# Kernel tuning notes

Hardware: AMD Instinct MI355X
Metric: run time of the kernel (lower is better)

The kernel has to match this reference:

```python
import jax, jax.numpy as jnp
import numpy as np

EPS = 1e-15

def gmm_conv(x, row, col, pseudo, g_w, mu, sigma, root_w, bias):
    # x: [N,Fin], pseudo: [E,D], g_w: [Fin,K*Fout], mu/sigma: [K,D], root_w: [Fin,Fout]
    N = x.shape[0]
    K, D = mu.shape
    Fout = g_w.shape[1] // K
    gx = (x @ g_w).reshape(N, K, Fout)                       # per-node kernel transforms
    diff = pseudo[:, None, :] - mu[None, :, :]               # [E,K,D]
    gauss = jnp.exp(-0.5 * jnp.sum(diff * diff / (EPS + sigma[None] ** 2), axis=-1))  # [E,K]
    msg = jnp.einsum('ek,eko->eo', gauss, gx[row])           # [E,Fout]
    agg = jax.ops.segment_sum(msg, col, num_segments=N)      # scatter-add to targets
    cnt = jax.ops.segment_sum(jnp.ones((msg.shape[0],), x.dtype), col, num_segments=N)
    agg = agg / jnp.maximum(cnt, 1.0)[:, None]               # mean aggregation (GMMConv default)
    return agg + x @ root_w + bias

def setup_inputs() -> dict:
    key = jax.random.key(0)
    ks = jax.random.split(key, 12)
    N, E, F, H, C, K, D = 50000, 800000, 128, 64, 16, 8, 2
    return {
        'x': jax.random.normal(ks[0], (N, F), jnp.float32),
        'edge_index': jax.random.randint(ks[1], (2, E), 0, N, jnp.int64),
        'edge_attr': jax.random.uniform(ks[2], (E, D), jnp.float32),
        'g1_w': jax.random.normal(ks[3], (F, K * H), jnp.float32) * 0.1,
        'mu1': jax.random.normal(ks[4], (K, D), jnp.float32),
        'sigma1': jax.random.uniform(ks[5], (K, D), jnp.float32) + 0.5,
        'root1_w': jax.random.normal(ks[6], (F, H), jnp.float32) * 0.1,
        'bias1': jnp.zeros((H,), jnp.float32),
        'g2_w': jax.random.normal(ks[7], (H, K * C), jnp.float32) * 0.1,
        'mu2': jax.random.normal(ks[8], (K, D), jnp.float32),
        'sigma2': jax.random.uniform(ks[9], (K, D), jnp.float32) + 0.5,
        'root2_w': jax.random.normal(ks[10], (H, C), jnp.float32) * 0.1,
        'bias2': jnp.zeros((C,), jnp.float32),
    }

def reference(x, edge_index, edge_attr, g1_w, mu1, sigma1, root1_w, bias1,
              g2_w, mu2, sigma2, root2_w, bias2):
    row, col = edge_index[0], edge_index[1]
    # dropout p applied in eval mode -> identity
    h = jax.nn.elu(gmm_conv(x, row, col, edge_attr, g1_w, mu1, sigma1, root1_w, bias1))
    out = gmm_conv(h, row, col, edge_attr, g2_w, mu2, sigma2, root2_w, bias2)
    return jax.nn.log_softmax(out, axis=1)
```

## Files before the change

kernel.cpp:

```cpp
#include <hip/hip_runtime.h>
#include <hip/hip_bf16.h>
#include <hip/hip_fp16.h>
#include <math.h>


#define NF 128
#define NH 64
#define NC 16
#define Z1NODES 16
#define Z1CAP 448
#define E2NODES 16
#define E2CAP 320
#define GXST 160

typedef __bf16 v8bf __attribute__((ext_vector_type(8)));
typedef float v4f __attribute__((ext_vector_type(4)));
typedef float v2f __attribute__((ext_vector_type(2)));

__device__ inline ushort f2bu(float x) {
  __hip_bfloat16 h = __float2bfloat16(x);
  return *(ushort*)&h;
}
__device__ inline uint packh2(float a, float b) {
  __half ha = __float2half_rn(a), hb = __float2half_rn(b);
  return (uint)(*(ushort*)&ha) | ((uint)(*(ushort*)&hb) << 16);
}
__device__ inline float2 unph2(uint u) {
  ushort a = (ushort)(u & 0xffff), b = (ushort)(u >> 16);
  return make_float2(__half2float(*(__half*)&a), __half2float(*(__half*)&b));
}
__device__ inline v8bf ld_frag(const ushort* p) {
  uint4 u = *(const uint4*)p;
  return __builtin_bit_cast(v8bf, u);
}
__device__ inline v2f fma2(float w, v2f f, v2f a) {
  return __builtin_elementwise_fma((v2f){w, w}, f, a);
}

__global__ __launch_bounds__(256) void setup_kernel(
    const int* __restrict__ col, const float* __restrict__ x,
    const float* __restrict__ g1w, const float* __restrict__ r1w,
    const float* __restrict__ g2w, const float* __restrict__ r2w,
    int* __restrict__ counts, ushort* __restrict__ A1,
    ushort* __restrict__ W1t, ushort* __restrict__ G2pT,
    int* __restrict__ bagg, int E, int N, int bh, int bc, int bp) {
  const int b = blockIdx.x, t = threadIdx.x;
  if (b < bh) {
    int e = b * 256 + t;
    if (e < E) atomicAdd(&counts[col[e]], 1);
  } else if (b < bh + bc) {
    int idx = (b - bh) * 256 + t;
    if (idx < N * 32) {
      int n = idx >> 5, c4 = idx & 31;
      float4 v = ((const float4*)x)[idx];
      ushort4 o;
      o.x = f2bu(v.x); o.y = f2bu(v.y); o.z = f2bu(v.z); o.w = f2bu(v.w);
      *(ushort4*)(A1 + (size_t)n * 1152 + 1024 + c4 * 4) = o;
    }
  } else if (b < bh + bc + bp) {
    int i = (b - bh - bc) * 256 + t;
    if (i < 64 * 1152) {
      int h = i / 1152, j = i % 1152;
      float v = (j < 1024) ? g1w[(size_t)(j & 127) * 512 + (j >> 7) * 64 + h]
                           : r1w[(size_t)(j - 1024) * 64 + h];
      W1t[i] = f2bu(v);
    } else {
      int i2 = i - 64 * 1152;
      if (i2 < 144 * 64) {
        int cp = i2 / 64, f = i2 % 64;
        float v;
        if (cp < 128) {
          int kq = cp >> 5, rem = cp & 31;
          int o = rem >> 1, k = kq * 2 + (rem & 1);
          v = g2w[(size_t)f * 128 + k * 16 + o];
        } else {
          v = r2w[(size_t)f * 16 + (cp - 128)];
        }
        G2pT[i2] = f2bu(v);
      }
    }
  } else {
    if (t < 64) bagg[t] = 0;
  }
}

__global__ __launch_bounds__(256) void scan_kernel(
    const int* __restrict__ counts, int* __restrict__ starts,
    int* __restrict__ cursor, int* __restrict__ bagg, int NB) {
  __shared__ int wsum[4];
  __shared__ int s_pre;
  const int t = threadIdx.x, lane = t & 63, wv = t >> 6;
  const int b = blockIdx.x;
  int4 v = ((const int4*)counts)[b * 256 + t];
  int tsum = v.x + v.y + v.z + v.w;
  int inc = tsum;
  #pragma unroll
  for (int off = 1; off < 64; off <<= 1) {
    int u = __shfl_up(inc, off, 64);
    if (lane >= off) inc += u;
  }
  if (lane == 63) wsum[wv] = inc;
  __syncthreads();
  int agg = wsum[0] + wsum[1] + wsum[2] + wsum[3];
  if (t == 0) atomicExch(&bagg[b], agg + 1);
  __threadfence();
  int pre = 0;
  if (wv == 0) {
    if (t < b) {
      int val;
      do { val = atomicAdd(&bagg[t], 0); } while (val == 0);
      pre = val - 1;
    }
    #pragma unroll
    for (int off = 32; off >= 1; off >>= 1) pre += __shfl_xor(pre, off, 64);
    if (lane == 0) s_pre = pre;
  }
  __syncthreads();
  int wpre = 0;
  for (int j = 0; j < wv; ++j) wpre += wsum[j];
  int excl = s_pre + wpre + inc - tsum;
  int4 o;
  o.x = excl; o.y = o.x + v.x; o.z = o.y + v.y; o.w = o.z + v.z;
  ((int4*)starts)[b * 256 + t] = o;
  ((int4*)cursor)[b * 256 + t] = o;
}

__global__ __launch_bounds__(256) void fill_kernel(
    const int* __restrict__ row, const int* __restrict__ col,
    const float* __restrict__ eattr,
    const float* __restrict__ mu1, const float* __restrict__ sg1,
    const float* __restrict__ mu2, const float* __restrict__ sg2,
    int* __restrict__ cursor, int* __restrict__ erow,
    uint4* __restrict__ ew1, uint4* __restrict__ ew2, int E) {
  int e = blockIdx.x * 256 + threadIdx.x;
  if (e >= E) return;
  int c = col[e];
  int pos = atomicAdd(&cursor[c], 1);
  float p0 = eattr[2 * e], p1 = eattr[2 * e + 1];
  float w1[8], w2[8];
  #pragma unroll
  for (int k = 0; k < 8; ++k) {
    float d0 = p0 - mu1[2 * k], d1 = p1 - mu1[2 * k + 1];
    float s0 = sg1[2 * k], s1 = sg1[2 * k + 1];
    w1[k] = __expf(-0.5f * (d0 * d0 / (1e-15f + s0 * s0) +
                            d1 * d1 / (1e-15f + s1 * s1)));
    float e0 = p0 - mu2[2 * k], e1 = p1 - mu2[2 * k + 1];
    float t0 = sg2[2 * k], t1 = sg2[2 * k + 1];
    w2[k] = __expf(-0.5f * (e0 * e0 / (1e-15f + t0 * t0) +
                            e1 * e1 / (1e-15f + t1 * t1)));
  }
  erow[pos] = row[e];
  ew1[pos] = make_uint4(packh2(w1[0], w1[1]), packh2(w1[2], w1[3]),
                        packh2(w1[4], w1[5]), packh2(w1[6], w1[7]));
  ew2[pos] = make_uint4(packh2(w2[0], w2[1]), packh2(w2[2], w2[3]),
                        packh2(w2[4], w2[5]), packh2(w2[6], w2[7]));
}

__global__ __launch_bounds__(256) void z1_kernel(
    ushort* __restrict__ A1, const int* __restrict__ erow,
    const uint4* __restrict__ ew1, const int* __restrict__ starts, int N) {
  __shared__ __align__(16) float lw[Z1CAP + 8][8];
  __shared__ int loff[Z1CAP + 8];
  const int t = threadIdx.x, lane = t & 63, wv = t >> 6;
  const int base = (int)blockIdx.x * Z1NODES;
  const int S = starts[base];
  const int cl = min(starts[base + Z1NODES] - S, Z1CAP);
  for (int i = t; i < cl; i += 256) {
    loff[i] = erow[S + i] * 2304;
    uint4 qq = ew1[S + i];
    float2 a = unph2(qq.x), b = unph2(qq.y), c = unph2(qq.z), d = unph2(qq.w);
    *(float4*)&lw[i][0] = make_float4(a.x, a.y, b.x, b.y);
    *(float4*)&lw[i][4] = make_float4(c.x, c.y, d.x, d.y);
  }
  if (t < 8) {
    loff[cl + t] = 0;
    *(float4*)&lw[cl + t][0] = make_float4(0.f, 0.f, 0.f, 0.f);
    *(float4*)&lw[cl + t][4] = make_float4(0.f, 0.f, 0.f, 0.f);
  }
  __syncthreads();

  const char* xb = (const char*)(A1 + 1024) + (lane << 2);

  for (int i = 0; i < Z1NODES / 4; ++i) {
    const int n = base + wv * 4 + i;
    const int be = starts[n], ee = starts[n + 1];
    v2f A[8];
    #pragma unroll
    for (int k = 0; k < 8; ++k) A[k] = (v2f){0.f, 0.f};

    const int reRel = min(ee - S, cl);
    for (int q = min(be - S, cl); q < reRel; q += 8) {
      int off[8];
      #pragma unroll
      for (int u = 0; u < 8; ++u) off[u] = loff[q + u];
      uint g[8];
      #pragma unroll
      for (int u = 0; u < 8; ++u) g[u] = *(const uint*)(xb + off[u]);
      #pragma unroll
      for (int u = 0; u < 8; ++u) {
        const bool ok = (q + u) < reRel;
        float4 wl = *(float4*)&lw[q + u][0];
        float4 wh = *(float4*)&lw[q + u][4];
        v2f F;
        F.x = ok ? __uint_as_float(g[u] << 16) : 0.f;
        F.y = ok ? __uint_as_float(g[u] & 0xffff0000u) : 0.f;
        A[0] = fma2(wl.x, F, A[0]);
        A[1] = fma2(wl.y, F, A[1]);
        A[2] = fma2(wl.z, F, A[2]);
        A[3] = fma2(wl.w, F, A[3]);
        A[4] = fma2(wh.x, F, A[4]);
        A[5] = fma2(wh.y, F, A[5]);
        A[6] = fma2(wh.z, F, A[6]);
        A[7] = fma2(wh.w, F, A[7]);
      }
    }
    for (int j = max(S + reRel, be); j < ee; ++j) {
      uint4 qq = ew1[j];
      uint g = *(const uint*)(xb + erow[j] * 2304);
      float2 a = unph2(qq.x), b = unph2(qq.y), c = unph2(qq.z), d = unph2(qq.w);
      v2f F;
      F.x = __uint_as_float(g << 16);
      F.y = __uint_as_float(g & 0xffff0000u);
      A[0] = fma2(a.x, F, A[0]); A[1] = fma2(a.y, F, A[1]);
      A[2] = fma2(b.x, F, A[2]); A[3] = fma2(b.y, F, A[3]);
      A[4] = fma2(c.x, F, A[4]); A[5] = fma2(c.y, F, A[5]);
      A[6] = fma2(d.x, F, A[6]); A[7] = fma2(d.y, F, A[7]);
    }
    const float inv = 1.f / fmaxf((float)(ee - be), 1.f);
    ushort* zr = A1 + (size_t)n * 1152;
    #pragma unroll
    for (int k = 0; k < 8; ++k) {
      uint pk = (uint)f2bu(A[k].x * inv) | ((uint)f2bu(A[k].y * inv) << 16);
      *(uint*)(zr + k * 128 + 2 * lane) = pk;
    }
  }
}

__global__ __launch_bounds__(256) void gemm12_kernel(
    const ushort* __restrict__ A1, const ushort* __restrict__ W1t,
    const float* __restrict__ b1, const ushort* __restrict__ G2pT,
    ushort* __restrict__ gx2e, int N) {
  __shared__ __align__(16) ushort As[2][64 * 32];
  __shared__ __align__(16) ushort Bs[2][64 * 32];
  __shared__ __align__(16) ushort Hs[64][72];
  const int t = threadIdx.x, lane = t & 63, wv = t >> 6;
  const int mfrag = lane & 15, quad = lane >> 4;
  const int m0 = (int)blockIdx.x * 64;
  const int st_r = t >> 2, st_c = (t & 3) * 8;
  const int st_o = st_r * 32 + st_c;
  const ushort* ag = A1 + (size_t)(m0 + st_r) * 1152 + st_c;
  const ushort* bg = W1t + (size_t)st_r * 1152 + st_c;

  {
    uint4 a0 = *(const uint4*)ag;
    uint4 b0 = *(const uint4*)bg;
    *(uint4*)(&As[0][st_o]) = a0;
    *(uint4*)(&Bs[0][st_o]) = b0;
  }
  __syncthreads();

  v4f acc[4];
  #pragma unroll
  for (int ct = 0; ct < 4; ++ct) acc[ct] = (v4f){0.f, 0.f, 0.f, 0.f};

  for (int kc = 0; kc < 36; ++kc) {
    const int cb = kc & 1, nb = cb ^ 1;
    uint4 an, bn;
    if (kc < 35) {
      an = *(const uint4*)(ag + (kc + 1) * 32);
      bn = *(const uint4*)(bg + (kc + 1) * 32);
    }
    v8bf a = ld_frag(&As[cb][(wv * 16 + mfrag) * 32 + quad * 8]);
    #pragma unroll
    for (int ct = 0; ct < 4; ++ct) {
      v8bf b = ld_frag(&Bs[cb][(ct * 16 + mfrag) * 32 + quad * 8]);
      acc[ct] = __builtin_amdgcn_mfma_f32_16x16x32_bf16(a, b, acc[ct], 0, 0, 0);
    }
    if (kc < 35) {
      *(uint4*)(&As[nb][st_o]) = an;
      *(uint4*)(&Bs[nb][st_o]) = bn;
      __syncthreads();
    }
  }
  #pragma unroll
  for (int ct = 0; ct < 4; ++ct) {
    const int colh = ct * 16 + mfrag;
    const float bc = b1[colh];
    #pragma unroll
    for (int r = 0; r < 4; ++r) {
      float v = acc[ct][r] + bc;
      v = v > 0.f ? v : expm1f(v);
      Hs[wv * 16 + quad * 4 + r][colh] = f2bu(v);
    }
  }
  __syncthreads();

  v4f acc2[9];
  #pragma unroll
  for (int t9 = 0; t9 < 9; ++t9) acc2[t9] = (v4f){0.f, 0.f, 0.f, 0.f};
  const ushort* brow = G2pT + (size_t)mfrag * 64 + quad * 8;
  #pragma unroll
  for (int kc = 0; kc < 2; ++kc) {
    v8bf a = ld_frag(&Hs[wv * 16 + mfrag][quad * 8 + kc * 32]);
    #pragma unroll
    for (int t9 = 0; t9 < 9; ++t9) {
      v8bf b = ld_frag(brow + (size_t)t9 * 16 * 64 + kc * 32);
      acc2[t9] = __builtin_amdgcn_mfma_f32_16x16x32_bf16(a, b, acc2[t9], 0, 0, 0);
    }
  }
  #pragma unroll
  for (int t9 = 0; t9 < 9; ++t9) {
    #pragma unroll
    for (int r = 0; r < 4; ++r) {
      int node = m0 + wv * 16 + quad * 4 + r;
      if (node < N)
        gx2e[(size_t)node * GXST + t9 * 16 + mfrag] = f2bu(acc2[t9][r]);
    }
  }
}

__global__ __launch_bounds__(256) void edge2_kernel(
    const ushort* __restrict__ gx2e, const int* __restrict__ erow,
    const uint4* __restrict__ ew2, const int* __restrict__ starts,
    const float* __restrict__ b2, float* __restrict__ out, int N) {
  __shared__ __align__(16) float lw[E2CAP + 8][8];
  __shared__ int loff[E2CAP + 8];
  __shared__ float lb2[16];
  const int t = threadIdx.x, lane = t & 63, wv = t >> 6;
  const int base = (int)blockIdx.x * E2NODES;
  const int S = starts[base];
  const int cl = min(starts[base + E2NODES] - S, E2CAP);
  if (t < 16) lb2[t] = b2[t];
  for (int i = t; i < cl; i += 256) {
    loff[i] = erow[S + i] * 320;
    uint4 qq = ew2[S + i];
    float2 a = unph2(qq.x), b = unph2(qq.y), c = unph2(qq.z), d = unph2(qq.w);
    *(float4*)&lw[i][0] = make_float4(a.x, a.y, b.x, b.y);
    *(float4*)&lw[i][4] = make_float4(c.x, c.y, d.x, d.y);
  }
  if (t < 8) {
    loff[cl + t] = 0;
    *(float4*)&lw[cl + t][0] = make_float4(0.f, 0.f, 0.f, 0.f);
    *(float4*)&lw[cl + t][4] = make_float4(0.f, 0.f, 0.f, 0.f);
  }
  __syncthreads();

  const int o = lane & 15, kq = lane >> 4;
  const char* gb = (const char*)gx2e + kq * 64 + o * 4;

  for (int i = 0; i < E2NODES / 4; ++i) {
    const int n = base + wv * 4 + i;
    if (n >= N) continue;
    const int be = starts[n], ee = starts[n + 1];
    v2f ACC = (v2f){0.f, 0.f};
    const int reRel = min(ee - S, cl);
    for (int q = min(be - S, cl); q < reRel; q += 8) {
      int off[8];
      #pragma unroll
      for (int u = 0; u < 8; ++u) off[u] = loff[q + u];
      uint g[8];
      #pragma unroll
      for (int u = 0; u < 8; ++u) g[u] = *(const uint*)(gb + off[u]);
      #pragma unroll
      for (int u = 0; u < 8; ++u) {
        const bool ok = (q + u) < reRel;
        v2f W = *(v2f*)&lw[q + u][kq * 2];
        v2f F;
        F.x = ok ? __uint_as_float(g[u] << 16) : 0.f;
        F.y = ok ? __uint_as_float(g[u] & 0xffff0000u) : 0.f;
        ACC = __builtin_elementwise_fma(W, F, ACC);
      }
    }
    for (int j = max(S + reRel, be); j < ee; ++j) {
      uint4 qq = ew2[j];
      uint comp = (kq == 0) ? qq.x : (kq == 1) ? qq.y : (kq == 2) ? qq.z : qq.w;
      float2 wp = unph2(comp);
      uint g = *(const uint*)(gb + erow[j] * 320);
      ACC.x = fmaf(wp.x, __uint_as_float(g << 16), ACC.x);
      ACC.y = fmaf(wp.y, __uint_as_float(g & 0xffff0000u), ACC.y);
    }
    float s = ACC.x + ACC.y;
    s += __shfl_xor(s, 16, 64);
    s += __shfl_xor(s, 32, 64);
    const float inv = 1.f / fmaxf((float)(ee - be), 1.f);
    ushort ru = *((const ushort*)gx2e + (size_t)n * GXST + 128 + o);
    float root = __uint_as_float(((uint)ru) << 16);
    float v = s * inv + root + lb2[o];
    float mx = v;
    #pragma unroll
    for (int off = 8; off >= 1; off >>= 1) mx = fmaxf(mx, __shfl_xor(mx, off, 64));
    float sm = __expf(v - mx);
    #pragma unroll
    for (int off = 8; off >= 1; off >>= 1) sm += __shfl_xor(sm, off, 64);
    if (kq == 0) out[(size_t)n * NC + o] = v - mx - __logf(sm);
  }
}

extern "C" void kernel_launch(void* const* d_in, const int* in_sizes, int n_in,
                              void* d_out, int out_size, void* d_ws, size_t ws_size,
                              hipStream_t stream) {
  const float* x     = (const float*)d_in[0];
  const int*   eidx  = (const int*)d_in[1];
  const float* eattr = (const float*)d_in[2];
  const float* g1w   = (const float*)d_in[3];
  const float* mu1   = (const float*)d_in[4];
  const float* sg1   = (const float*)d_in[5];
  const float* r1w   = (const float*)d_in[6];
  const float* b1    = (const float*)d_in[7];
  const float* g2w   = (const float*)d_in[8];
  const float* mu2   = (const float*)d_in[9];
  const float* sg2   = (const float*)d_in[10];
  const float* r2w   = (const float*)d_in[11];
  const float* b2    = (const float*)d_in[12];

  const int N = in_sizes[0] / NF;
  const int E = in_sizes[1] / 2;
  const int* row = eidx;
  const int* col = eidx + E;
  const int N2 = (N + 63) & ~63;
  const int NP = (N + 1023) & ~1023;
  const int NB = NP / 1024;

  char* wsb = (char*)d_ws;
  uint4* ew2   = (uint4*)wsb;
  uint4* ew1   = (uint4*)(wsb + (size_t)E * 16);
  ushort* gx2e = (ushort*)ew1;
  size_t ew1span = (size_t)N2 * 320;
  if (ew1span < (size_t)E * 16) ew1span = (size_t)E * 16;
  ushort* A1   = (ushort*)(wsb + (size_t)E * 16 + ew1span);
  ushort* W1t  = A1 + (size_t)N2 * 1152;
  ushort* G2pT = W1t + (size_t)64 * 1152;
  int* erow    = (int*)(G2pT + (size_t)144 * 64);
  int* counts  = erow + (size_t)E;
  int* starts  = counts + NP;
  int* cursor  = starts + NP;
  int* bagg    = cursor + NP;

  const int bh = (E + 255) / 256;
  const int bc = (N * 32 + 255) / 256;
  const int bp = (64 * 1152 + 144 * 64 + 255) / 256;

  hipMemsetAsync(counts, 0, (size_t)NP * sizeof(int), stream);
  setup_kernel<<<bh + bc + bp + 1, 256, 0, stream>>>(
      col, x, g1w, r1w, g2w, r2w, counts, A1, W1t, G2pT, bagg, E, N, bh, bc, bp);
  scan_kernel<<<NB, 256, 0, stream>>>(counts, starts, cursor, bagg, NB);
  fill_kernel<<<bh, 256, 0, stream>>>(row, col, eattr, mu1, sg1, mu2, sg2,
                                      cursor, erow, ew1, ew2, E);
  z1_kernel<<<N / Z1NODES, 256, 0, stream>>>(A1, erow, ew1, starts, N);
  gemm12_kernel<<<N2 / 64, 256, 0, stream>>>(A1, W1t, b1, G2pT, gx2e, N);
  edge2_kernel<<<(N + E2NODES - 1) / E2NODES, 256, 0, stream>>>(
      gx2e, erow, ew2, starts, b2, (float*)d_out, N);
}
```

Before: 334.6 us.

## Record edge rank in histogram pass and recompute gaussian weights in consumers

The histogram pass now stores each edge's atomic rank, so the fill pass places edges at starts[col]+rank without a second atomic on a cursor array. Fill writes one 16-byte record per edge holding precomputed row offsets for both layers and the raw pseudo-coordinates, instead of separate erow plus two fp16 weight arrays. The z1 and edge2 kernels recompute the 8 gaussian weights on the fly from shared-memory mu/sigma constants. This trades extra exp work in the aggregation kernels for less edge-array traffic and one fewer atomic pass, and keeps the weights in fp32 instead of fp16.

```diff
diff --git a/kernel.cpp b/kernel.cpp
--- a/kernel.cpp
+++ b/kernel.cpp
@@ -21,14 +21,6 @@
   __hip_bfloat16 h = __float2bfloat16(x);
   return *(ushort*)&h;
 }
-__device__ inline uint packh2(float a, float b) {
-  __half ha = __float2half_rn(a), hb = __float2half_rn(b);
-  return (uint)(*(ushort*)&ha) | ((uint)(*(ushort*)&hb) << 16);
-}
-__device__ inline float2 unph2(uint u) {
-  ushort a = (ushort)(u & 0xffff), b = (ushort)(u >> 16);
-  return make_float2(__half2float(*(__half*)&a), __half2float(*(__half*)&b));
-}
 __device__ inline v8bf ld_frag(const ushort* p) {
   uint4 u = *(const uint4*)p;
   return __builtin_bit_cast(v8bf, u);
@@ -41,13 +33,14 @@
     const int* __restrict__ col, const float* __restrict__ x,
     const float* __restrict__ g1w, const float* __restrict__ r1w,
     const float* __restrict__ g2w, const float* __restrict__ r2w,
-    int* __restrict__ counts, ushort* __restrict__ A1,
-    ushort* __restrict__ W1t, ushort* __restrict__ G2pT,
-    int* __restrict__ bagg, int E, int N, int bh, int bc, int bp) {
+    int* __restrict__ counts, int* __restrict__ rank,
+    ushort* __restrict__ A1, ushort* __restrict__ W1t,
+    ushort* __restrict__ G2pT, int* __restrict__ bagg,
+    int E, int N, int bh, int bc, int bp) {
   const int b = blockIdx.x, t = threadIdx.x;
   if (b < bh) {
     int e = b * 256 + t;
-    if (e < E) atomicAdd(&counts[col[e]], 1);
+    if (e < E) rank[e] = atomicAdd(&counts[col[e]], 1);
   } else if (b < bh + bc) {
     int idx = (b - bh) * 256 + t;
     if (idx < N * 32) {
@@ -86,7 +79,7 @@
 
 __global__ __launch_bounds__(256) void scan_kernel(
     const int* __restrict__ counts, int* __restrict__ starts,
-    int* __restrict__ cursor, int* __restrict__ bagg, int NB) {
+    int* __restrict__ bagg, int NB) {
   __shared__ int wsum[4];
   __shared__ int s_pre;
   const int t = threadIdx.x, lane = t & 63, wv = t >> 6;
@@ -122,55 +115,52 @@
   int4 o;
   o.x = excl; o.y = o.x + v.x; o.z = o.y + v.y; o.w = o.z + v.z;
   ((int4*)starts)[b * 256 + t] = o;
-  ((int4*)cursor)[b * 256 + t] = o;
-}
-
-__global__ __launch_bounds__(256) void fill_kernel(
+}
+
+__global__ __launch_bounds__(256) void fillrec_kernel(
     const int* __restrict__ row, const int* __restrict__ col,
-    const float* __restrict__ eattr,
-    const float* __restrict__ mu1, const float* __restrict__ sg1,
-    const float* __restrict__ mu2, const float* __restrict__ sg2,
-    int* __restrict__ cursor, int* __restrict__ erow,
-    uint4* __restrict__ ew1, uint4* __restrict__ ew2, int E) {
+    const int* __restrict__ rank, const int* __restrict__ starts,
+    const float* __restrict__ eattr, uint4* __restrict__ rec, int E) {
   int e = blockIdx.x * 256 + threadIdx.x;
   if (e >= E) return;
-  int c = col[e];
-  int pos = atomicAdd(&cursor[c], 1);
-  float p0 = eattr[2 * e], p1 = eattr[2 * e + 1];
-  float w1[8], w2[8];
-  #pragma unroll
-  for (int k = 0; k < 8; ++k) {
-    float d0 = p0 - mu1[2 * k], d1 = p1 - mu1[2 * k + 1];
-    float s0 = sg1[2 * k], s1 = sg1[2 * k + 1];
-    w1[k] = __expf(-0.5f * (d0 * d0 / (1e-15f + s0 * s0) +
-                            d1 * d1 / (1e-15f + s1 * s1)));
-    float e0 = p0 - mu2[2 * k], e1 = p1 - mu2[2 * k + 1];
-    float t0 = sg2[2 * k], t1 = sg2[2 * k + 1];
-    w2[k] = __expf(-0.5f * (e0 * e0 / (1e-15f + t0 * t0) +
-                            e1 * e1 / (1e-15f + t1 * t1)));
-  }
-  erow[pos] = row[e];
-  ew1[pos] = make_uint4(packh2(w1[0], w1[1]), packh2(w1[2], w1[3]),
-                        packh2(w1[4], w1[5]), packh2(w1[6], w1[7]));
-  ew2[pos] = make_uint4(packh2(w2[0], w2[1]), packh2(w2[2], w2[3]),
-                        packh2(w2[4], w2[5]), packh2(w2[6], w2[7]));
+  int pos = starts[col[e]] + rank[e];
+  int r = row[e];
+  float2 p = *(const float2*)(eattr + 2 * e);
+  rec[pos] = make_uint4((uint)(r * 2304), __float_as_uint(p.x),
+                        __float_as_uint(p.y), (uint)(r * 320));
 }
 
 __global__ __launch_bounds__(256) void z1_kernel(
-    ushort* __restrict__ A1, const int* __restrict__ erow,
-    const uint4* __restrict__ ew1, const int* __restrict__ starts, int N) {
+    ushort* __restrict__ A1, const uint4* __restrict__ rec,
+    const float* __restrict__ mu1, const float* __restrict__ sg1,
+    const int* __restrict__ starts, int N) {
   __shared__ __align__(16) float lw[Z1CAP + 8][8];
   __shared__ int loff[Z1CAP + 8];
+  __shared__ float prm[32];
   const int t = threadIdx.x, lane = t & 63, wv = t >> 6;
   const int base = (int)blockIdx.x * Z1NODES;
   const int S = starts[base];
   const int cl = min(starts[base + Z1NODES] - S, Z1CAP);
+  if (t < 8) {
+    float s0 = sg1[2 * t], s1 = sg1[2 * t + 1];
+    prm[t] = -0.5f / (1e-15f + s0 * s0);
+    prm[8 + t] = -0.5f / (1e-15f + s1 * s1);
+    prm[16 + t] = mu1[2 * t];
+    prm[24 + t] = mu1[2 * t + 1];
+  }
+  __syncthreads();
   for (int i = t; i < cl; i += 256) {
-    loff[i] = erow[S + i] * 2304;
-    uint4 qq = ew1[S + i];
-    float2 a = unph2(qq.x), b = unph2(qq.y), c = unph2(qq.z), d = unph2(qq.w);
-    *(float4*)&lw[i][0] = make_float4(a.x, a.y, b.x, b.y);
-    *(float4*)&lw[i][4] = make_float4(c.x, c.y, d.x, d.y);
+    uint4 rr = rec[S + i];
+    loff[i] = (int)rr.x;
+    float p0 = __uint_as_float(rr.y), p1 = __uint_as_float(rr.z);
+    float w[8];
+    #pragma unroll
+    for (int k = 0; k < 8; ++k) {
+      float d0 = p0 - prm[16 + k], d1 = p1 - prm[24 + k];
+      w[k] = __expf(fmaf(d0 * d0, prm[k], d1 * d1 * prm[8 + k]));
+    }
+    *(float4*)&lw[i][0] = make_float4(w[0], w[1], w[2], w[3]);
+    *(float4*)&lw[i][4] = make_float4(w[4], w[5], w[6], w[7]);
   }
   if (t < 8) {
     loff[cl + t] = 0;
@@ -215,16 +205,18 @@
       }
     }
     for (int j = max(S + reRel, be); j < ee; ++j) {
-      uint4 qq = ew1[j];
-      uint g = *(const uint*)(xb + erow[j] * 2304);
-      float2 a = unph2(qq.x), b = unph2(qq.y), c = unph2(qq.z), d = unph2(qq.w);
+      uint4 rr = rec[j];
+      uint g = *(const uint*)(xb + (int)rr.x);
+      float p0 = __uint_as_float(rr.y), p1 = __uint_as_float(rr.z);
       v2f F;
       F.x = __uint_as_float(g << 16);
       F.y = __uint_as_float(g & 0xffff0000u);
-      A[0] = fma2(a.x, F, A[0]); A[1] = fma2(a.y, F, A[1]);
-      A[2] = fma2(b.x, F, A[2]); A[3] = fma2(b.y, F, A[3]);
-      A[4] = fma2(c.x, F, A[4]); A[5] = fma2(c.y, F, A[5]);
-      A[6] = fma2(d.x, F, A[6]); A[7] = fma2(d.y, F, A[7]);
+      #pragma unroll
+      for (int k = 0; k < 8; ++k) {
+        float d0 = p0 - prm[16 + k], d1 = p1 - prm[24 + k];
+        float w = __expf(fmaf(d0 * d0, prm[k], d1 * d1 * prm[8 + k]));
+        A[k] = fma2(w, F, A[k]);
+      }
     }
     const float inv = 1.f / fmaxf((float)(ee - be), 1.f);
     ushort* zr = A1 + (size_t)n * 1152;
@@ -320,23 +312,39 @@
 }
 
 __global__ __launch_bounds__(256) void edge2_kernel(
-    const ushort* __restrict__ gx2e, const int* __restrict__ erow,
-    const uint4* __restrict__ ew2, const int* __restrict__ starts,
-    const float* __restrict__ b2, float* __restrict__ out, int N) {
+    const ushort* __restrict__ gx2e, const uint4* __restrict__ rec,
+    const float* __restrict__ mu2, const float* __restrict__ sg2,
+    const int* __restrict__ starts, const float* __restrict__ b2,
+    float* __restrict__ out, int N) {
   __shared__ __align__(16) float lw[E2CAP + 8][8];
   __shared__ int loff[E2CAP + 8];
   __shared__ float lb2[16];
+  __shared__ float prm[32];
   const int t = threadIdx.x, lane = t & 63, wv = t >> 6;
   const int base = (int)blockIdx.x * E2NODES;
   const int S = starts[base];
   const int cl = min(starts[base + E2NODES] - S, E2CAP);
   if (t < 16) lb2[t] = b2[t];
+  if (t < 8) {
+    float s0 = sg2[2 * t], s1 = sg2[2 * t + 1];
+    prm[t] = -0.5f / (1e-15f + s0 * s0);
+    prm[8 + t] = -0.5f / (1e-15f + s1 * s1);
+    prm[16 + t] = mu2[2 * t];
+    prm[24 + t] = mu2[2 * t + 1];
+  }
+  __syncthreads();
   for (int i = t; i < cl; i += 256) {
-    loff[i] = erow[S + i] * 320;
-    uint4 qq = ew2[S + i];
-    float2 a = unph2(qq.x), b = unph2(qq.y), c = unph2(qq.z), d = unph2(qq.w);
-    *(float4*)&lw[i][0] = make_float4(a.x, a.y, b.x, b.y);
-    *(float4*)&lw[i][4] = make_float4(c.x, c.y, d.x, d.y);
+    uint4 rr = rec[S + i];
+    loff[i] = (int)rr.w;
+    float p0 = __uint_as_float(rr.y), p1 = __uint_as_float(rr.z);
+    float w[8];
+    #pragma unroll
+    for (int k = 0; k < 8; ++k) {
+      float d0 = p0 - prm[16 + k], d1 = p1 - prm[24 + k];
+      w[k] = __expf(fmaf(d0 * d0, prm[k], d1 * d1 * prm[8 + k]));
+    }
+    *(float4*)&lw[i][0] = make_float4(w[0], w[1], w[2], w[3]);
+    *(float4*)&lw[i][4] = make_float4(w[4], w[5], w[6], w[7]);
   }
   if (t < 8) {
     loff[cl + t] = 0;
@@ -372,12 +380,16 @@
       }
     }
     for (int j = max(S + reRel, be); j < ee; ++j) {
-      uint4 qq = ew2[j];
-      uint comp = (kq == 0) ? qq.x : (kq == 1) ? qq.y : (kq == 2) ? qq.z : qq.w;
-      float2 wp = unph2(comp);
-      uint g = *(const uint*)(gb + erow[j] * 320);
-      ACC.x = fmaf(wp.x, __uint_as_float(g << 16), ACC.x);
-      ACC.y = fmaf(wp.y, __uint_as_float(g & 0xffff0000u), ACC.y);
+      uint4 rr = rec[j];
+      uint g = *(const uint*)(gb + (int)rr.w);
+      float p0 = __uint_as_float(rr.y), p1 = __uint_as_float(rr.z);
+      float d00 = p0 - prm[16 + 2 * kq], d01 = p1 - prm[24 + 2 * kq];
+      float d10 = p0 - prm[16 + 2 * kq + 1], d11 = p1 - prm[24 + 2 * kq + 1];
+      float w0 = __expf(fmaf(d00 * d00, prm[2 * kq], d01 * d01 * prm[8 + 2 * kq]));
+      float w1 = __expf(fmaf(d10 * d10, prm[2 * kq + 1],
+                             d11 * d11 * prm[8 + 2 * kq + 1]));
+      ACC.x = fmaf(w0, __uint_as_float(g << 16), ACC.x);
+      ACC.y = fmaf(w1, __uint_as_float(g & 0xffff0000u), ACC.y);
     }
     float s = ACC.x + ACC.y;
     s += __shfl_xor(s, 16, 64);
@@ -422,19 +434,15 @@
   const int NB = NP / 1024;
 
   char* wsb = (char*)d_ws;
-  uint4* ew2   = (uint4*)wsb;
-  uint4* ew1   = (uint4*)(wsb + (size_t)E * 16);
-  ushort* gx2e = (ushort*)ew1;
-  size_t ew1span = (size_t)N2 * 320;
-  if (ew1span < (size_t)E * 16) ew1span = (size_t)E * 16;
-  ushort* A1   = (ushort*)(wsb + (size_t)E * 16 + ew1span);
+  uint4* rec   = (uint4*)wsb;
+  ushort* gx2e = (ushort*)(wsb + (size_t)E * 16);
+  ushort* A1   = gx2e + (size_t)N2 * GXST;
   ushort* W1t  = A1 + (size_t)N2 * 1152;
   ushort* G2pT = W1t + (size_t)64 * 1152;
-  int* erow    = (int*)(G2pT + (size_t)144 * 64);
-  int* counts  = erow + (size_t)E;
+  int* rank    = (int*)(G2pT + (size_t)144 * 64);
+  int* counts  = rank + (size_t)E;
   int* starts  = counts + NP;
-  int* cursor  = starts + NP;
-  int* bagg    = cursor + NP;
+  int* bagg    = starts + NP;
 
   const int bh = (E + 255) / 256;
   const int bc = (N * 32 + 255) / 256;
@@ -442,12 +450,12 @@
 
   hipMemsetAsync(counts, 0, (size_t)NP * sizeof(int), stream);
   setup_kernel<<<bh + bc + bp + 1, 256, 0, stream>>>(
-      col, x, g1w, r1w, g2w, r2w, counts, A1, W1t, G2pT, bagg, E, N, bh, bc, bp);
-  scan_kernel<<<NB, 256, 0, stream>>>(counts, starts, cursor, bagg, NB);
-  fill_kernel<<<bh, 256, 0, stream>>>(row, col, eattr, mu1, sg1, mu2, sg2,
-                                      cursor, erow, ew1, ew2, E);
-  z1_kernel<<<N / Z1NODES, 256, 0, stream>>>(A1, erow, ew1, starts, N);
+      col, x, g1w, r1w, g2w, r2w, counts, rank, A1, W1t, G2pT, bagg,
+      E, N, bh, bc, bp);
+  scan_kernel<<<NB, 256, 0, stream>>>(counts, starts, bagg, NB);
+  fillrec_kernel<<<bh, 256, 0, stream>>>(row, col, rank, starts, eattr, rec, E);
+  z1_kernel<<<N / Z1NODES, 256, 0, stream>>>(A1, rec, mu1, sg1, starts, N);
   gemm12_kernel<<<N2 / 64, 256, 0, stream>>>(A1, W1t, b1, G2pT, gx2e, N);
   edge2_kernel<<<(N + E2NODES - 1) / E2NODES, 256, 0, stream>>>(
-      gx2e, erow, ew2, starts, b2, (float*)d_out, N);
-}
+      gx2e, rec, mu2, sg2, starts, b2, (float*)d_out, N);
+}
```

After: 287.5 us. 14.1% less time.
